# Kernel tuning notes

Measured on AMD Instinct MI355X. Metric: run time of the kernel, lower is better.

The kernel has to match this reference:

```python
import jax, jax.numpy as jnp
import numpy as np

N_NODES = 50000
N_EDGES = 800000
IN_CH = 128
HIDDEN = 64
LATENT = 64
OUT_CH = 128
N_GRAPHS = 500
NEG_SLOPE = 0.2


def _gat_layer(x, src, dst, W, a_src, a_dst, b, n_nodes):
    """PyG GATConv (heads=1, concat=True, add_self_loops=True, edge_dim=None)."""
    h = x @ W  # [N, F]
    loops = jnp.arange(n_nodes)
    s = jnp.concatenate([src, loops])  # source (j) of each edge incl. self loops
    d = jnp.concatenate([dst, loops])  # destination (i)
    score_src = h @ a_src  # [N]
    score_dst = h @ a_dst  # [N]
    alpha = jax.nn.leaky_relu(score_src[s] + score_dst[d], NEG_SLOPE)  # [E+N]
    # softmax grouped by destination node
    amax = jax.ops.segment_max(alpha, d, num_segments=n_nodes)
    e = jnp.exp(alpha - amax[d])
    denom = jax.ops.segment_sum(e, d, num_segments=n_nodes)
    coef = e / (denom[d] + 1e-16)
    out = jax.ops.segment_sum(h[s] * coef[:, None], d, num_segments=n_nodes)
    return out + b


def setup_inputs() -> dict:
    key = jax.random.key(0)
    ks = jax.random.split(key, 24)
    g = lambda k, shape, fan: jax.random.normal(k, shape, jnp.float32) * (1.0 / np.sqrt(fan))
    inp = {
        "x": jax.random.normal(ks[0], (N_NODES, IN_CH), jnp.float32),
        "edge_index": jax.random.randint(ks[1], (2, N_EDGES), 0, N_NODES, dtype=jnp.int64),
        "batch": jnp.sort(jax.random.randint(ks[2], (N_NODES,), 0, N_GRAPHS, dtype=jnp.int64)),
        "edge_attr": jax.random.normal(ks[3], (N_EDGES, 3), jnp.float32),
        # conv1 (GATConv in->hidden)
        "W1": g(ks[4], (IN_CH, HIDDEN), IN_CH),
        "a_src1": g(ks[5], (HIDDEN,), HIDDEN),
        "a_dst1": g(ks[6], (HIDDEN,), HIDDEN),
        "b1": jnp.zeros((HIDDEN,), jnp.float32),
        # conv2 (GATConv hidden->latent)
        "W2": g(ks[7], (HIDDEN, LATENT), HIDDEN),
        "a_src2": g(ks[8], (LATENT,), LATENT),
        "a_dst2": g(ks[9], (LATENT,), LATENT),
        "b2": jnp.zeros((LATENT,), jnp.float32),
        # encoder linear
        "lin_W": g(ks[10], (LATENT, LATENT), LATENT),
        "lin_b": jnp.zeros((LATENT,), jnp.float32),
        # decoder x_mlp
        "xm_W1": g(ks[11], (LATENT, HIDDEN), LATENT),
        "xm_b1": jnp.zeros((HIDDEN,), jnp.float32),
        "xm_W2": g(ks[12], (HIDDEN, OUT_CH), HIDDEN),
        "xm_b2": jnp.zeros((OUT_CH,), jnp.float32),
        # decoder edge_mlp
        "em_W1": g(ks[13], (LATENT, HIDDEN), LATENT),
        "em_b1": jnp.zeros((HIDDEN,), jnp.float32),
        "em_W2": g(ks[14], (HIDDEN, 3), HIDDEN),
        "em_b2": jnp.zeros((3,), jnp.float32),
    }
    return inp


def reference(x, edge_index, batch, edge_attr,
              W1, a_src1, a_dst1, b1,
              W2, a_src2, a_dst2, b2,
              lin_W, lin_b,
              xm_W1, xm_b1, xm_W2, xm_b2,
              em_W1, em_b1, em_W2, em_b2):
    src, dst = edge_index[0], edge_index[1]
    n = x.shape[0]
    # Encoder (eval mode: dropout is identity; edge_attr unused since edge_dim=None)
    h = _gat_layer(x, src, dst, W1, a_src1, a_dst1, b1, n)
    h = jax.nn.relu(h)
    z = _gat_layer(h, src, dst, W2, a_src2, a_dst2, b2, n)
    z = z @ lin_W + lin_b
    # global_mean_pool over batch ids
    sums = jax.ops.segment_sum(z, batch, num_segments=N_GRAPHS)
    counts = jax.ops.segment_sum(jnp.ones((n,), z.dtype), batch, num_segments=N_GRAPHS)
    graph_embedding = sums / jnp.maximum(counts, 1.0)[:, None]
    # MLP decoders
    x_hat = jax.nn.relu(z @ xm_W1 + xm_b1) @ xm_W2 + xm_b2
    e_hat = jax.nn.relu(z @ em_W1 + em_b1) @ em_W2 + em_b2
    return (x_hat, e_hat, z, graph_embedding)
```

## Files before the change

kernel.cpp:

```cpp
#include <hip/hip_runtime.h>
#include <hip/hip_bf16.h>
#include <cstring>

#define N_NODES 50000
#define N_EDGES 800000
#define IN_CH 128
#define NG 500
#define OUT_ELEMS 9782000
#define NBUCK 196
#define BCAP 8192
#define CSRCAP (NBUCK * BCAP)
#define GEMMB 3125
#define DECB 3125

using bf16 = __hip_bfloat16;
typedef unsigned short u16;
typedef unsigned int u32;
typedef long long i64;
typedef unsigned long long u64;

__device__ __forceinline__ float b2f(bf16 v) { return __bfloat162float(v); }
__device__ __forceinline__ float tofl(float v) { return v; }
__device__ __forceinline__ float tofl(bf16 v) { return __bfloat162float(v); }
__device__ __forceinline__ float ldflt(const void* p, int i, int f32) {
  return f32 ? ((const float*)p)[i] : b2f(((const bf16*)p)[i]);
}
__device__ __forceinline__ int ldedge(const void* p, int i, int is64) {
  return is64 ? (int)((const i64*)p)[i] : ((const int*)p)[i];
}
__device__ __forceinline__ float sane(float v) {
  if (!isfinite(v)) return 0.f;
  return fminf(fmaxf(v, -65504.f), 65504.f);
}
__device__ __forceinline__ float lrelu(float x) { return x > 0.f ? x : 0.2f * x; }
__device__ __forceinline__ float bflo(u32 u) { return __uint_as_float(u << 16); }
__device__ __forceinline__ float bfhi(u32 u) { return __uint_as_float(u & 0xffff0000u); }

__device__ __forceinline__ float wsum(float v) {
#pragma unroll
  for (int o = 32; o > 0; o >>= 1) v += __shfl_xor(v, o, 64);
  return v;
}


__global__ void fillsig_kernel(float* __restrict__ out, int n, float v) {
  int i = blockIdx.x * 256 + threadIdx.x;
  if (i < n) out[i] = v;
}

__global__ void zero_kernel(int* __restrict__ p, int n) {
  int i = threadIdx.x;
  if (i < n) p[i] = 0;
}

#define BCHUNK 4096

template <int FIN, typename FT>
__device__ void gemm16_compute(float (&xl)[16][FIN], const void* Wv, const void* asv,
                               const void* adv, bf16* __restrict__ h, float* __restrict__ ss,
                               float* __restrict__ sd, int rbase) {
  const FT* W = (const FT*)Wv;
  const FT* as_ = (const FT*)asv;
  const FT* ad_ = (const FT*)adv;
  int lane = threadIdx.x & 63, w = threadIdx.x >> 6;
  float a_s = tofl(as_[lane]), a_d = tofl(ad_[lane]);
  int r0 = w * 4;
  float acc0 = 0.f, acc1 = 0.f, acc2 = 0.f, acc3 = 0.f;
  for (int k = 0; k < FIN; ++k) {
    float wk = tofl(W[k * 64 + lane]);
    acc0 = fmaf(xl[r0 + 0][k], wk, acc0);
    acc1 = fmaf(xl[r0 + 1][k], wk, acc1);
    acc2 = fmaf(xl[r0 + 2][k], wk, acc2);
    acc3 = fmaf(xl[r0 + 3][k], wk, acc3);
  }
  float acc[4] = {sane(acc0), sane(acc1), sane(acc2), sane(acc3)};
#pragma unroll
  for (int j = 0; j < 4; ++j) {
    int g = rbase + r0 + j;
    h[g * 64 + lane] = __float2bfloat16(acc[j]);
    float vs = wsum(acc[j] * a_s);
    float vd = wsum(acc[j] * a_d);
    if (lane == 0) { ss[g] = sane(vs); sd[g] = sane(vd); }
  }
}

__global__ __launch_bounds__(256) void bucket_gemm_kernel(
    const void* __restrict__ ei, int* __restrict__ bcnt, u32* __restrict__ tmp,
    const void* __restrict__ xin, const void* __restrict__ W, const void* __restrict__ asrc,
    const void* __restrict__ adst, int* __restrict__ fl, bf16* __restrict__ h,
    float* __restrict__ ss, float* __restrict__ sd) {
  __shared__ int hist[NBUCK], run[NBUCK], gbase[NBUCK];
  __shared__ float xl[16][IN_CH];
  __shared__ int cs;
  int bid = blockIdx.x, tid = threadIdx.x;
  if (bid < NBUCK) {
    if (tid == 0) cs = 0;
    if (tid < NBUCK) { hist[tid] = 0; run[tid] = 0; }
    __syncthreads();
    const int* e32 = (const int*)ei;
    atomicAdd(&cs, (e32[2 * tid + 1] == 0) ? 1 : 0);
    __syncthreads();
    int is64 = cs > 128;
    int base = bid * BCHUNK;
#pragma unroll
    for (int k = 0; k < 16; ++k) {
      int e = base + k * 256 + tid;
      if (e < N_EDGES) {
        unsigned d = (unsigned)ldedge(ei, N_EDGES + e, is64);
        if (d < N_NODES) atomicAdd(&hist[d >> 8], 1);
      }
    }
    __syncthreads();
    if (tid < NBUCK) {
      int hh = hist[tid];
      gbase[tid] = hh ? atomicAdd(&bcnt[tid], hh) : 0;
    }
    __syncthreads();
#pragma unroll
    for (int k = 0; k < 16; ++k) {
      int e = base + k * 256 + tid;
      if (e < N_EDGES) {
        unsigned d = (unsigned)ldedge(ei, N_EDGES + e, is64);
        if (d < N_NODES) {
          unsigned s = (unsigned)ldedge(ei, e, is64);
          if (s >= N_NODES) s = 0;
          int t = d >> 8;
          int pl = gbase[t] + atomicAdd(&run[t], 1);
          if (pl < BCAP) tmp[t * BCAP + pl] = (s << 8) | (d & 255u);
        }
      }
    }
    return;
  }
  if (bid < NBUCK + 2) {
    if (tid == 0) cs = 0;
    __syncthreads();
    int cnt = 0;
    if (bid == NBUCK) {
      const u16* xb = (const u16*)xin;
#pragma unroll 4
      for (int k = 0; k < 32; ++k) {
        int i = tid + 256 * k;
        u16 u = xb[2 * i];
        int e = (u >> 7) & 0xFF;
        if (e != 0 && (e < 90 || e > 150)) ++cnt;
      }
    } else {
      const int* e32 = (const int*)ei;
#pragma unroll 4
      for (int k = 0; k < 32; ++k) {
        int i = tid + 256 * k;
        if (e32[2 * i + 1] == 0) ++cnt;
      }
    }
    atomicAdd(&cs, cnt);
    __syncthreads();
    if (tid == 0) fl[bid == NBUCK ? 7 : 6] = cs;
    return;
  }
  if (tid == 0) cs = 0;
  __syncthreads();
  {
    const u16* xb = (const u16*)xin;
    u16 u = xb[2 * tid];
    int e = (u >> 7) & 0xFF;
    atomicAdd(&cs, (e != 0 && (e < 90 || e > 150)) ? 1 : 0);
  }
  __syncthreads();
  int wf = cs > 64;
  int rbase = (bid - NBUCK - 2) * 16;
  for (int i = tid; i < 16 * IN_CH; i += 256) {
    int rr = i / IN_CH, cc = i % IN_CH;
    xl[rr][cc] = ldflt(xin, (rbase + rr) * IN_CH + cc, wf);
  }
  __syncthreads();
  if (wf)
    gemm16_compute<IN_CH, float>(xl, W, asrc, adst, h, ss, sd, rbase);
  else
    gemm16_compute<IN_CH, bf16>(xl, W, asrc, adst, h, ss, sd, rbase);
}

__global__ __launch_bounds__(1024) void scatter2c_kernel(const u32* __restrict__ tmp,
                                                         const int* __restrict__ bcnt,
                                                         int* __restrict__ offs,
                                                         int* __restrict__ ends,
                                                         int* __restrict__ csr) {
  __shared__ int lcnt[256], lex[256], lcur[256];
  int b = blockIdx.x;
  int tid = threadIdx.x;
  if (tid < 256) { lcnt[tid] = 0; lcur[tid] = 0; }
  __syncthreads();
  int nodelo = b << 8;
  int cnt = min(bcnt[b], BCAP);
  int tbase = b * BCAP;
  for (int i = tid; i < cnt; i += 1024) {
    int li = (int)(tmp[tbase + i] & 255u);
    atomicAdd(&lcnt[li], 1);
  }
  __syncthreads();
  if (tid < 256) lex[tid] = lcnt[tid];
  __syncthreads();
  for (int off = 1; off < 256; off <<= 1) {
    int add = (tid < 256 && tid >= off) ? lex[tid - off] : 0;
    __syncthreads();
    if (tid < 256) lex[tid] += add;
    __syncthreads();
  }
  if (tid < 256) {
    int ex = lex[tid] - lcnt[tid];
    lex[tid] = ex;
    int node = nodelo + tid;
    if (node < N_NODES) {
      offs[node] = tbase + ex;
      ends[node] = tbase + ex + lcnt[tid];
    }
  }
  __syncthreads();
  for (int i = tid; i < cnt; i += 1024) {
    u32 v = tmp[tbase + i];
    int li = (int)(v & 255u);
    int s = (int)(v >> 8);
    int pos = tbase + lex[li] + atomicAdd(&lcur[li], 1);
    if (pos < CSRCAP) csr[pos] = s;
  }
}

__device__ __forceinline__ float2 agg_node2(const bf16* __restrict__ h,
                                            const float* __restrict__ ss,
                                            const float* __restrict__ sd,
                                            const int* __restrict__ offs,
                                            const int* __restrict__ ends,
                                            const int* __restrict__ csr, int d, int lane) {
  int hl = lane & 31;
  int hbase = lane & 32;
  float sdd = sd[d];
  int beg = offs[d], end = ends[d];
  beg = max(0, min(beg, CSRCAP));
  end = max(beg, min(end, CSRCAP));
  float wself = __expf(fminf(lrelu(ss[d] + sdd), 60.f));
  u32 uself = ((const u32*)h)[d * 32 + hl];
  float2 acc;
  acc.x = bflo(uself) * wself;
  acc.y = bfhi(uself) * wself;
  float dpart = (hl == 0) ? wself : 0.f;
  for (int cb = beg; cb < end; cb += 32) {
    int j = cb + hl;
    int s = 0;
    float wv = 0.f;
    if (j < end) {
      s = csr[j];
      s = ((unsigned)s < N_NODES) ? s : 0;
      wv = __expf(fminf(lrelu(ss[s] + sdd), 60.f));
    }
    dpart += wv;
    int cnt = min(32, end - cb);
    for (int t0 = 0; t0 < cnt; t0 += 16) {
      u32 hv[16];
#pragma unroll
      for (int q = 0; q < 16; ++q) {
        int sq = __shfl(s, hbase + t0 + q, 64);
        hv[q] = ((const u32*)h)[sq * 32 + hl];
      }
#pragma unroll
      for (int q = 0; q < 16; ++q) {
        float wq = __shfl(wv, hbase + t0 + q, 64);
        acc.x = fmaf(bflo(hv[q]), wq, acc.x);
        acc.y = fmaf(bfhi(hv[q]), wq, acc.y);
      }
    }
  }
#pragma unroll
  for (int o = 16; o > 0; o >>= 1) dpart += __shfl_xor(dpart, o, 64);
  float den = dpart + 1e-16f;
  acc.x = acc.x / den;
  acc.y = acc.y / den;
  return acc;
}

template <typename FT>
__device__ void gemm2_compute(float (&xl)[8][64], int r0, const void* Wv, const void* asv,
                              const void* adv, bf16* __restrict__ h, float* __restrict__ ss,
                              float* __restrict__ sd, int rbase) {
  const FT* W = (const FT*)Wv;
  const FT* as_ = (const FT*)asv;
  const FT* ad_ = (const FT*)adv;
  int lane = threadIdx.x & 63;
  float a_s = tofl(as_[lane]), a_d = tofl(ad_[lane]);
  float acc0 = 0.f, acc1 = 0.f;
  for (int k = 0; k < 64; ++k) {
    float wk = tofl(W[k * 64 + lane]);
    acc0 = fmaf(xl[r0 + 0][k], wk, acc0);
    acc1 = fmaf(xl[r0 + 1][k], wk, acc1);
  }
  float acc[2] = {sane(acc0), sane(acc1)};
#pragma unroll
  for (int j = 0; j < 2; ++j) {
    int g = rbase + r0 + j;
    h[g * 64 + lane] = __float2bfloat16(acc[j]);
    float vs = wsum(acc[j] * a_s);
    float vd = wsum(acc[j] * a_d);
    if (lane == 0) { ss[g] = sane(vs); sd[g] = sane(vd); }
  }
}

template <typename FT>
__device__ void lin2_compute(float (&xl)[8][64], int r0, const void* Wv, const void* bv,
                             float* __restrict__ zio, int rbase) {
  const FT* W = (const FT*)Wv;
  const FT* b = (const FT*)bv;
  int lane = threadIdx.x & 63;
  float bl = tofl(b[lane]);
  float acc0 = bl, acc1 = bl;
  for (int k = 0; k < 64; ++k) {
    float wk = tofl(W[k * 64 + lane]);
    acc0 = fmaf(xl[r0 + 0][k], wk, acc0);
    acc1 = fmaf(xl[r0 + 1][k], wk, acc1);
  }
  float acc[2] = {sane(acc0), sane(acc1)};
#pragma unroll
  for (int j = 0; j < 2; ++j) zio[(rbase + r0 + j) * 64 + lane] = acc[j];
}

__global__ __launch_bounds__(256) void agg_gemm_kernel(
    const bf16* __restrict__ hL, const float* __restrict__ ssL, const float* __restrict__ sdL,
    const int* __restrict__ offs, const int* __restrict__ ends, const int* __restrict__ csr,
    const void* __restrict__ bias, const int* __restrict__ fl, const void* __restrict__ W2,
    const void* __restrict__ as2, const void* __restrict__ ad2, bf16* __restrict__ hOut,
    float* __restrict__ ssOut, float* __restrict__ sdOut) {
  __shared__ float o1l[8][64];
  int wf = fl[7] > 2000;
  int lane = threadIdx.x & 63, w = threadIdx.x >> 6;
  int hl = lane & 31, half = lane >> 5;
  int rbase = blockIdx.x * 8;
  int d = rbase + 2 * w + half;
  float2 r = agg_node2(hL, ssL, sdL, offs, ends, csr, d, lane);
  float blx = ldflt(bias, 2 * hl, wf), bly = ldflt(bias, 2 * hl + 1, wf);
  o1l[2 * w + half][2 * hl] = sane(fmaxf(r.x + blx, 0.f));
  o1l[2 * w + half][2 * hl + 1] = sane(fmaxf(r.y + bly, 0.f));
  __syncthreads();
  if (wf)
    gemm2_compute<float>(o1l, 2 * w, W2, as2, ad2, hOut, ssOut, sdOut, rbase);
  else
    gemm2_compute<bf16>(o1l, 2 * w, W2, as2, ad2, hOut, ssOut, sdOut, rbase);
}

__global__ __launch_bounds__(256) void agg_lin_kernel(
    const bf16* __restrict__ hL, const float* __restrict__ ssL, const float* __restrict__ sdL,
    const int* __restrict__ offs, const int* __restrict__ ends, const int* __restrict__ csr,
    const void* __restrict__ bias, const int* __restrict__ fl, const void* __restrict__ linW,
    const void* __restrict__ linb, float* __restrict__ zreg) {
  __shared__ float o2l[8][64];
  int wf = fl[7] > 2000;
  int lane = threadIdx.x & 63, w = threadIdx.x >> 6;
  int hl = lane & 31, half = lane >> 5;
  int rbase = blockIdx.x * 8;
  int d = rbase + 2 * w + half;
  float2 r = agg_node2(hL, ssL, sdL, offs, ends, csr, d, lane);
  float blx = ldflt(bias, 2 * hl, wf), bly = ldflt(bias, 2 * hl + 1, wf);
  o2l[2 * w + half][2 * hl] = sane(r.x + blx);
  o2l[2 * w + half][2 * hl + 1] = sane(r.y + bly);
  __syncthreads();
  if (wf)
    lin2_compute<float>(o2l, 2 * w, linW, linb, zreg, rbase);
  else
    lin2_compute<bf16>(o2l, 2 * w, linW, linb, zreg, rbase);
}

template <typename FT>
__device__ void dec16_compute(float (&zl)[16][64], float (&t1x)[16][64], float (&t1e)[16][65],
                              float (&W2l)[192], const void* xW1v, const void* xb1v,
                              const void* xW2v, const void* xb2v, const void* eW1v,
                              const void* eb1v, const void* eb2v, float* __restrict__ xout,
                              float* __restrict__ eout, int rbase) {
  const FT* xW1 = (const FT*)xW1v;
  const FT* xb1 = (const FT*)xb1v;
  const FT* xW2 = (const FT*)xW2v;
  const FT* xb2 = (const FT*)xb2v;
  const FT* eW1 = (const FT*)eW1v;
  const FT* eb1 = (const FT*)eb1v;
  const FT* eb2 = (const FT*)eb2v;
  int lane = threadIdx.x & 63, w = threadIdx.x >> 6;
  int r0 = w * 4;
  {
    float bx = tofl(xb1[lane]), be = tofl(eb1[lane]);
    float x0 = bx, x1 = bx, x2 = bx, x3 = bx;
    float e0 = be, e1 = be, e2 = be, e3 = be;
    for (int k = 0; k < 64; ++k) {
      float z0 = zl[r0 + 0][k], z1 = zl[r0 + 1][k];
      float z2 = zl[r0 + 2][k], z3 = zl[r0 + 3][k];
      float wx = tofl(xW1[k * 64 + lane]);
      float we = tofl(eW1[k * 64 + lane]);
      x0 = fmaf(z0, wx, x0);
      x1 = fmaf(z1, wx, x1);
      x2 = fmaf(z2, wx, x2);
      x3 = fmaf(z3, wx, x3);
      e0 = fmaf(z0, we, e0);
      e1 = fmaf(z1, we, e1);
      e2 = fmaf(z2, we, e2);
      e3 = fmaf(z3, we, e3);
    }
    t1x[r0 + 0][lane] = fmaxf(x0, 0.f);
    t1x[r0 + 1][lane] = fmaxf(x1, 0.f);
    t1x[r0 + 2][lane] = fmaxf(x2, 0.f);
    t1x[r0 + 3][lane] = fmaxf(x3, 0.f);
    t1e[r0 + 0][lane] = fmaxf(e0, 0.f);
    t1e[r0 + 1][lane] = fmaxf(e1, 0.f);
    t1e[r0 + 2][lane] = fmaxf(e2, 0.f);
    t1e[r0 + 3][lane] = fmaxf(e3, 0.f);
  }
  {
    float b2a = tofl(xb2[lane]), b2b = tofl(xb2[64 + lane]);
    float a0[4] = {b2a, b2a, b2a, b2a};
    float a1[4] = {b2b, b2b, b2b, b2b};
    for (int k = 0; k < 64; ++k) {
      float wa = tofl(xW2[k * 128 + lane]);
      float wb = tofl(xW2[k * 128 + 64 + lane]);
#pragma unroll
      for (int j = 0; j < 4; ++j) {
        float tv = t1x[r0 + j][k];
        a0[j] = fmaf(tv, wa, a0[j]);
        a1[j] = fmaf(tv, wb, a1[j]);
      }
    }
#pragma unroll
    for (int j = 0; j < 4; ++j) {
      int g = rbase + r0 + j;
      xout[g * 128 + lane] = sane(a0[j]);
      xout[g * 128 + 64 + lane] = sane(a1[j]);
    }
  }
  {
    int j = lane >> 4, c = lane & 15;
    if (c < 3) {
      int row = r0 + j;
      float acc = tofl(eb2[c]);
#pragma unroll 4
      for (int k = 0; k < 64; ++k) acc = fmaf(t1e[row][k], W2l[k * 3 + c], acc);
      eout[(rbase + row) * 3 + c] = sane(acc);
    }
  }
}

__global__ __launch_bounds__(256) void dec_pool_kernel(
    const float* __restrict__ z, const void* __restrict__ xmW1, const void* __restrict__ xmb1,
    const void* __restrict__ xmW2, const void* __restrict__ xmb2, const void* __restrict__ emW1,
    const void* __restrict__ emb1, const void* __restrict__ emW2, const void* __restrict__ emb2,
    const void* __restrict__ batch, const int* __restrict__ fl, float* __restrict__ xout,
    float* __restrict__ eout, float* __restrict__ emb) {
  __shared__ float zl[16][64];
  __shared__ float t1x[16][64];
  __shared__ float t1e[16][65];
  __shared__ float W2l[192];
  int tid = threadIdx.x;
  if (blockIdx.x < NG) {
    float(&sm)[4][64] = *reinterpret_cast<float(*)[4][64]>(&zl[0][0]);
    int* bounds = (int*)&t1x[0][0];
    int g = blockIdx.x;
    int lane = tid & 63, w = tid >> 6;
    int is64 = fl[6] > 4000;
    if (tid < 2) {
      int target = g + tid;
      int lo = 0, hi = N_NODES;
      while (lo < hi) {
        int mid = (lo + hi) >> 1;
        if (ldedge(batch, mid, is64) < target) lo = mid + 1; else hi = mid;
      }
      bounds[tid] = lo;
    }
    __syncthreads();
    int beg = bounds[0], end = bounds[1];
    float acc = 0.f;
    for (int r = beg + w; r < end; r += 4) acc += z[r * 64 + lane];
    sm[w][lane] = acc;
    __syncthreads();
    if (w == 0) {
      float v = sm[0][lane] + sm[1][lane] + sm[2][lane] + sm[3][lane];
      float cnt = (float)max(end - beg, 1);
      emb[g * 64 + lane] = sane(v / cnt);
    }
    return;
  }
  int wf = fl[7] > 2000;
  int rbase = (blockIdx.x - NG) * 16;
  for (int i = tid; i < 1024; i += 256) zl[i >> 6][i & 63] = z[rbase * 64 + i];
  if (tid < 192) W2l[tid] = wf ? ((const float*)emW2)[tid] : b2f(((const bf16*)emW2)[tid]);
  __syncthreads();
  if (wf)
    dec16_compute<float>(zl, t1x, t1e, W2l, xmW1, xmb1, xmW2, xmb2, emW1, emb1, emb2,
                         xout, eout, rbase);
  else
    dec16_compute<bf16>(zl, t1x, t1e, W2l, xmW1, xmb1, xmW2, xmb2, emW1, emb1, emb2,
                        xout, eout, rbase);
}

extern "C" void kernel_launch(void* const* d_in, const int* in_sizes, int n_in,
                              void* d_out, int out_size, void* d_ws, size_t ws_size,
                              hipStream_t stream) {
  float* outf = (float*)d_out;
  if (out_size != OUT_ELEMS) {
    float sig = 2048.0f + fminf((float)out_size * 1e-4f, 999.f);
    fillsig_kernel<<<(out_size + 255) / 256, 256, 0, stream>>>(outf, out_size, sig);
    return;
  }
  if (n_in < 22 || in_sizes[0] != N_NODES * IN_CH || in_sizes[1] != 2 * N_EDGES) {
    fillsig_kernel<<<(out_size + 255) / 256, 256, 0, stream>>>(outf, out_size, 5000.f);
    return;
  }

  const void* x = d_in[0];
  const void* ei = d_in[1];
  const void* batch = d_in[2];
  const void* W1 = d_in[4];
  const void* as1 = d_in[5];
  const void* ad1 = d_in[6];
  const void* b1 = d_in[7];
  const void* W2 = d_in[8];
  const void* as2 = d_in[9];
  const void* ad2 = d_in[10];
  const void* b2 = d_in[11];
  const void* linW = d_in[12];
  const void* linb = d_in[13];
  const void* xmW1 = d_in[14];
  const void* xmb1 = d_in[15];
  const void* xmW2 = d_in[16];
  const void* xmb2 = d_in[17];
  const void* emW1 = d_in[18];
  const void* emb1 = d_in[19];
  const void* emW2 = d_in[20];
  const void* emb2 = d_in[21];

  float* xhat = outf;
  float* ehat = outf + 6400000;
  float* zreg = outf + 6550000;
  float* emb = outf + 9750000;

  bool usews = ws_size >= (size_t)20500000;
  char* base = usews ? (char*)d_ws : (char*)d_out;
  int* bcnt = (int*)(base + 0);
  int* flags = (int*)(base + 800);
  int* offs = (int*)(base + 1024);
  int* ends = (int*)(base + 201024);
  float* ssb = (float*)(base + 401024);
  float* sdb = (float*)(base + 601024);
  int* csr = (int*)(base + 801024);
  bf16* hbuf = (bf16*)(base + 7223552);
  u32* tmp = (u32*)(base + 13623552);
  float* ss2 = (float*)(base + 13623552);
  float* sd2 = (float*)(base + 13823552);
  bf16* hbuf2 = (bf16*)(base + 14023552);

  int err = 0, idx = 0;
  (void)hipGetLastError();
#define CK()                                                                       \
  do {                                                                             \
    ++idx;                                                                         \
    hipError_t e_ = hipGetLastError();                                             \
    if (e_ != hipSuccess && err == 0) err = 8192 + idx * 256 + ((int)e_ & 3) * 64; \
  } while (0)

  zero_kernel<<<1, 256, 0, stream>>>(bcnt, 200); CK();
  bucket_gemm_kernel<<<NBUCK + 2 + GEMMB, 256, 0, stream>>>(
      ei, bcnt, tmp, x, W1, as1, ad1, flags, hbuf, ssb, sdb); CK();
  scatter2c_kernel<<<NBUCK, 1024, 0, stream>>>(tmp, bcnt, offs, ends, csr); CK();
  agg_gemm_kernel<<<N_NODES / 8, 256, 0, stream>>>(hbuf, ssb, sdb, offs, ends, csr, b1,
                                                   flags, W2, as2, ad2, hbuf2, ss2, sd2); CK();
  agg_lin_kernel<<<N_NODES / 8, 256, 0, stream>>>(hbuf2, ss2, sd2, offs, ends, csr, b2,
                                                  flags, linW, linb, zreg); CK();
  dec_pool_kernel<<<NG + DECB, 256, 0, stream>>>(zreg, xmW1, xmb1, xmW2, xmb2,
                                                 emW1, emb1, emW2, emb2, batch, flags,
                                                 xhat, ehat, emb); CK();
#undef CK

  if (err != 0) {
    static float s_sent;
    s_sent = (float)err;
    (void)hipMemcpyAsync(d_out, &s_sent, 4, hipMemcpyHostToDevice, stream);
  }
}
```

Before: 287.8 us.

## Fuse second-layer aggregation with linear and decoder MLPs; separate segment pooling

Fuses the encoder linear layer and both decoder MLPs into the second GAT aggregation kernel, keeping z and the hidden activations in shared memory rather than reloading z from global memory in a separate decoder kernel. Mean pooling moves to a small per-graph kernel that binary-searches the sorted batch ids to get its segment bounds. The zero kernel becomes a hipMemsetAsync. In exchange the fused kernel is heavier and uses more shared memory per block, which may lower occupancy, and the fused path runs only when usews is set.

```diff
diff --git a/kernel.cpp b/kernel.cpp
--- a/kernel.cpp
+++ b/kernel.cpp
@@ -46,11 +46,6 @@
 __global__ void fillsig_kernel(float* __restrict__ out, int n, float v) {
   int i = blockIdx.x * 256 + threadIdx.x;
   if (i < n) out[i] = v;
-}
-
-__global__ void zero_kernel(int* __restrict__ p, int n) {
-  int i = threadIdx.x;
-  if (i < n) p[i] = 0;
 }
 
 #define BCHUNK 4096
@@ -342,6 +337,153 @@
     gemm2_compute<float>(o1l, 2 * w, W2, as2, ad2, hOut, ssOut, sdOut, rbase);
   else
     gemm2_compute<bf16>(o1l, 2 * w, W2, as2, ad2, hOut, ssOut, sdOut, rbase);
+}
+
+template <typename FT>
+__device__ void lin_dec2_compute(float (&o2l)[8][64], float (&zl)[8][64],
+                                 float (&t1x)[8][64], float (&t1e)[8][65], float (&W2l)[192],
+                                 const void* linWv, const void* linbv, const void* xW1v,
+                                 const void* xb1v, const void* xW2v, const void* xb2v,
+                                 const void* eW1v, const void* eb1v, const void* eb2v,
+                                 float* __restrict__ zreg, float* __restrict__ xout,
+                                 float* __restrict__ eout, int rbase) {
+  const FT* linW = (const FT*)linWv;
+  const FT* linb = (const FT*)linbv;
+  const FT* xW1 = (const FT*)xW1v;
+  const FT* xb1 = (const FT*)xb1v;
+  const FT* xW2 = (const FT*)xW2v;
+  const FT* xb2 = (const FT*)xb2v;
+  const FT* eW1 = (const FT*)eW1v;
+  const FT* eb1 = (const FT*)eb1v;
+  const FT* eb2 = (const FT*)eb2v;
+  int lane = threadIdx.x & 63, w = threadIdx.x >> 6;
+  int r0 = 2 * w;
+  {
+    float bl = tofl(linb[lane]);
+    float acc0 = bl, acc1 = bl;
+    for (int k = 0; k < 64; ++k) {
+      float wk = tofl(linW[k * 64 + lane]);
+      acc0 = fmaf(o2l[r0 + 0][k], wk, acc0);
+      acc1 = fmaf(o2l[r0 + 1][k], wk, acc1);
+    }
+    float z0 = sane(acc0), z1 = sane(acc1);
+    zreg[(rbase + r0 + 0) * 64 + lane] = z0;
+    zreg[(rbase + r0 + 1) * 64 + lane] = z1;
+    zl[r0 + 0][lane] = z0;
+    zl[r0 + 1][lane] = z1;
+  }
+  {
+    float bx = tofl(xb1[lane]), be = tofl(eb1[lane]);
+    float x0 = bx, x1 = bx, e0 = be, e1 = be;
+    for (int k = 0; k < 64; ++k) {
+      float z0 = zl[r0 + 0][k], z1 = zl[r0 + 1][k];
+      float wx = tofl(xW1[k * 64 + lane]);
+      float we = tofl(eW1[k * 64 + lane]);
+      x0 = fmaf(z0, wx, x0);
+      x1 = fmaf(z1, wx, x1);
+      e0 = fmaf(z0, we, e0);
+      e1 = fmaf(z1, we, e1);
+    }
+    t1x[r0 + 0][lane] = fmaxf(x0, 0.f);
+    t1x[r0 + 1][lane] = fmaxf(x1, 0.f);
+    t1e[r0 + 0][lane] = fmaxf(e0, 0.f);
+    t1e[r0 + 1][lane] = fmaxf(e1, 0.f);
+  }
+  {
+    float b2a = tofl(xb2[lane]), b2b = tofl(xb2[64 + lane]);
+    float a0[2] = {b2a, b2a};
+    float a1[2] = {b2b, b2b};
+    for (int k = 0; k < 64; ++k) {
+      float wa = tofl(xW2[k * 128 + lane]);
+      float wb = tofl(xW2[k * 128 + 64 + lane]);
+#pragma unroll
+      for (int j = 0; j < 2; ++j) {
+        float tv = t1x[r0 + j][k];
+        a0[j] = fmaf(tv, wa, a0[j]);
+        a1[j] = fmaf(tv, wb, a1[j]);
+      }
+    }
+#pragma unroll
+    for (int j = 0; j < 2; ++j) {
+      int g = rbase + r0 + j;
+      xout[g * 128 + lane] = sane(a0[j]);
+      xout[g * 128 + 64 + lane] = sane(a1[j]);
+    }
+  }
+  {
+    int j = lane >> 5, c = lane & 31;
+    if (c < 3) {
+      int row = r0 + j;
+      float acc = tofl(eb2[c]);
+#pragma unroll 4
+      for (int k = 0; k < 64; ++k) acc = fmaf(t1e[row][k], W2l[k * 3 + c], acc);
+      eout[(rbase + row) * 3 + c] = sane(acc);
+    }
+  }
+}
+
+__global__ __launch_bounds__(256) void agg_lin_dec_kernel(
+    const bf16* __restrict__ hL, const float* __restrict__ ssL, const float* __restrict__ sdL,
+    const int* __restrict__ offs, const int* __restrict__ ends, const int* __restrict__ csr,
+    const void* __restrict__ bias, const int* __restrict__ fl, const void* __restrict__ linW,
+    const void* __restrict__ linb, const void* __restrict__ xmW1, const void* __restrict__ xmb1,
+    const void* __restrict__ xmW2, const void* __restrict__ xmb2, const void* __restrict__ emW1,
+    const void* __restrict__ emb1, const void* __restrict__ emW2, const void* __restrict__ emb2,
+    float* __restrict__ zreg, float* __restrict__ xout, float* __restrict__ eout) {
+  __shared__ float o2l[8][64];
+  __shared__ float zl[8][64];
+  __shared__ float t1x[8][64];
+  __shared__ float t1e[8][65];
+  __shared__ float W2l[192];
+  int wf = fl[7] > 2000;
+  int tid = threadIdx.x;
+  int lane = tid & 63, w = tid >> 6;
+  int hl = lane & 31, half = lane >> 5;
+  int rbase = blockIdx.x * 8;
+  if (tid < 192) W2l[tid] = wf ? ((const float*)emW2)[tid] : b2f(((const bf16*)emW2)[tid]);
+  int d = rbase + 2 * w + half;
+  float2 r = agg_node2(hL, ssL, sdL, offs, ends, csr, d, lane);
+  float blx = ldflt(bias, 2 * hl, wf), bly = ldflt(bias, 2 * hl + 1, wf);
+  o2l[2 * w + half][2 * hl] = sane(r.x + blx);
+  o2l[2 * w + half][2 * hl + 1] = sane(r.y + bly);
+  __syncthreads();
+  if (wf)
+    lin_dec2_compute<float>(o2l, zl, t1x, t1e, W2l, linW, linb, xmW1, xmb1, xmW2, xmb2,
+                            emW1, emb1, emb2, zreg, xout, eout, rbase);
+  else
+    lin_dec2_compute<bf16>(o2l, zl, t1x, t1e, W2l, linW, linb, xmW1, xmb1, xmW2, xmb2,
+                           emW1, emb1, emb2, zreg, xout, eout, rbase);
+}
+
+__global__ __launch_bounds__(256) void pool_seg_kernel(const float* __restrict__ z,
+                                                       const void* __restrict__ batch,
+                                                       const int* __restrict__ fl,
+                                                       float* __restrict__ emb) {
+  __shared__ float sm[4][64];
+  __shared__ int bounds[2];
+  int g = blockIdx.x;
+  int tid = threadIdx.x, lane = tid & 63, w = tid >> 6;
+  int is64 = fl[6] > 4000;
+  if (tid < 2) {
+    int target = g + tid;
+    int lo = 0, hi = N_NODES;
+    while (lo < hi) {
+      int mid = (lo + hi) >> 1;
+      if (ldedge(batch, mid, is64) < target) lo = mid + 1; else hi = mid;
+    }
+    bounds[tid] = lo;
+  }
+  __syncthreads();
+  int beg = bounds[0], end = bounds[1];
+  float acc = 0.f;
+  for (int r = beg + w; r < end; r += 4) acc += z[r * 64 + lane];
+  sm[w][lane] = acc;
+  __syncthreads();
+  if (w == 0) {
+    float v = sm[0][lane] + sm[1][lane] + sm[2][lane] + sm[3][lane];
+    float cnt = (float)max(end - beg, 1);
+    emb[g * 64 + lane] = sane(v / cnt);
+  }
 }
 
 __global__ __launch_bounds__(256) void agg_lin_kernel(
@@ -558,17 +700,24 @@
     if (e_ != hipSuccess && err == 0) err = 8192 + idx * 256 + ((int)e_ & 3) * 64; \
   } while (0)
 
-  zero_kernel<<<1, 256, 0, stream>>>(bcnt, 200); CK();
+  (void)hipMemsetAsync(bcnt, 0, 800, stream); CK();
   bucket_gemm_kernel<<<NBUCK + 2 + GEMMB, 256, 0, stream>>>(
       ei, bcnt, tmp, x, W1, as1, ad1, flags, hbuf, ssb, sdb); CK();
   scatter2c_kernel<<<NBUCK, 1024, 0, stream>>>(tmp, bcnt, offs, ends, csr); CK();
   agg_gemm_kernel<<<N_NODES / 8, 256, 0, stream>>>(hbuf, ssb, sdb, offs, ends, csr, b1,
                                                    flags, W2, as2, ad2, hbuf2, ss2, sd2); CK();
-  agg_lin_kernel<<<N_NODES / 8, 256, 0, stream>>>(hbuf2, ss2, sd2, offs, ends, csr, b2,
-                                                  flags, linW, linb, zreg); CK();
-  dec_pool_kernel<<<NG + DECB, 256, 0, stream>>>(zreg, xmW1, xmb1, xmW2, xmb2,
-                                                 emW1, emb1, emW2, emb2, batch, flags,
-                                                 xhat, ehat, emb); CK();
+  if (usews) {
+    agg_lin_dec_kernel<<<N_NODES / 8, 256, 0, stream>>>(
+        hbuf2, ss2, sd2, offs, ends, csr, b2, flags, linW, linb,
+        xmW1, xmb1, xmW2, xmb2, emW1, emb1, emW2, emb2, zreg, xhat, ehat); CK();
+    pool_seg_kernel<<<NG, 256, 0, stream>>>(zreg, batch, flags, emb); CK();
+  } else {
+    agg_lin_kernel<<<N_NODES / 8, 256, 0, stream>>>(hbuf2, ss2, sd2, offs, ends, csr, b2,
+                                                    flags, linW, linb, zreg); CK();
+    dec_pool_kernel<<<NG + DECB, 256, 0, stream>>>(zreg, xmW1, xmb1, xmW2, xmb2,
+                                                   emW1, emb1, emW2, emb2, batch, flags,
+                                                   xhat, ehat, emb); CK();
+  }
 #undef CK
 
   if (err != 0) {
```

Result: slower. 303.8 us (+5.5%).
